# Kernel tuning notes

Hardware: AMD Instinct MI355X
Metric: run time of the kernel (lower is better)

Reference implementation:

```python
import jax, jax.numpy as jnp
import numpy as np

MX, MY, MZ = 16, 16, 8  # modes_x, modes_y, modes_z
B, S1, S2, S3, I = 4, 64, 64, 40, 32
HID = 2 * I  # factor * dim


def setup_inputs() -> dict:
    key = jax.random.key(0)
    ks = jax.random.split(key, 14)
    s = 0.05
    d = {}
    d["x"] = jax.random.normal(ks[0], (B, S1, S2, S3, I), jnp.float32)
    # 1x1 Conv1d (in_dim -> in_dim)
    d["w_weight"] = jax.random.normal(ks[1], (I, I), jnp.float32) * s
    d["w_bias"] = jax.random.normal(ks[2], (I,), jnp.float32) * s
    # fourier_weight (positive-mode blocks), stored as (..., 2) real/imag like torch
    d["fw_xy"] = jax.random.normal(ks[3], (I, I, MX, MY, 2), jnp.float32) * s
    d["fw_yz"] = jax.random.normal(ks[4], (I, I, MY, MZ, 2), jnp.float32) * s
    d["fw_xz"] = jax.random.normal(ks[5], (I, I, MX, MZ, 2), jnp.float32) * s
    # fourier_weight2 (negative-mode blocks)
    d["fw2_xy"] = jax.random.normal(ks[6], (I, I, MX, MY, 2), jnp.float32) * s
    d["fw2_yz"] = jax.random.normal(ks[7], (I, I, MY, MZ, 2), jnp.float32) * s
    d["fw2_xz"] = jax.random.normal(ks[8], (I, I, MX, MZ, 2), jnp.float32) * s
    # backcast FeedForward: Linear(I->2I), ReLU, Linear(2I->I)
    d["ff_w0"] = jax.random.normal(ks[9], (HID, I), jnp.float32) * s
    d["ff_b0"] = jax.random.normal(ks[10], (HID,), jnp.float32) * s
    d["ff_w1"] = jax.random.normal(ks[11], (I, HID), jnp.float32) * s
    d["ff_b1"] = jax.random.normal(ks[12], (I,), jnp.float32) * s
    return d


def _cplx(w):
    return w[..., 0] + 1j * w[..., 1]


def _forward_fourier(x, w_weight, w_bias, fw_xy, fw_yz, fw_xz, fw2_xy, fw2_yz, fw2_xz):
    xt = jnp.transpose(x, (0, 4, 1, 2, 3))  # b i x y z
    b_, i_, s1, s2, s3 = xt.shape
    # 1x1 conv branch
    x_w = jnp.einsum('oi,bixyz->boxyz', w_weight, xt) + w_bias[None, :, None, None, None]
    # --- xz branch: rfftn over (x, z), real axis = z ---
    ft = jnp.fft.rfftn(xt, axes=(-3, -1))          # (b,i,s1,s2,s3//2+1)
    Z = s3 // 2 + 1
    out = jnp.zeros(ft.shape, ft.dtype)
    out = out.at[:, :, :MX, :, :MZ].set(
        jnp.einsum('bixyz,ioxz->boxyz', ft[:, :, :MX, :, :MZ], _cplx(fw_xz)))
    out = out.at[:, :, :MX, :, Z - MZ:].set(
        jnp.einsum('bixyz,ioxz->boxyz', ft[:, :, :MX, :, Z - MZ:], _cplx(fw2_xz)))
    xz = jnp.fft.irfftn(out, s=(s1, s3), axes=(-3, -1))
    # --- yz branch: rfftn over (y, z), real axis = z ---
    ft = jnp.fft.rfftn(xt, axes=(-2, -1))          # (b,i,s1,s2,s3//2+1)
    out = jnp.zeros(ft.shape, ft.dtype)
    out = out.at[:, :, :, :MY, :MZ].set(
        jnp.einsum('bixyz,ioyz->boxyz', ft[:, :, :, :MY, :MZ], _cplx(fw_yz)))
    out = out.at[:, :, :, :MY, Z - MZ:].set(
        jnp.einsum('bixyz,ioyz->boxyz', ft[:, :, :, :MY, Z - MZ:], _cplx(fw2_yz)))
    yz = jnp.fft.irfftn(out, s=(s2, s3), axes=(-2, -1))
    # --- xy branch: rfftn over (x, y), real axis = y ---
    ft = jnp.fft.rfftn(xt, axes=(-3, -2))          # (b,i,s1,s2//2+1,s3)
    Y = s2 // 2 + 1
    out = jnp.zeros(ft.shape, ft.dtype)
    out = out.at[:, :, :MX, :MY, :].set(
        jnp.einsum('bixyz,ioxy->boxyz', ft[:, :, :MX, :MY, :], _cplx(fw_xy)))
    out = out.at[:, :, :MX, Y - MY:, :].set(
        jnp.einsum('bixyz,ioxy->boxyz', ft[:, :, :MX, Y - MY:, :], _cplx(fw2_xy)))
    xy = jnp.fft.irfftn(out, s=(s1, s2), axes=(-3, -2))
    total = xy + yz + xz + x_w
    return jnp.transpose(total, (0, 2, 3, 4, 1))  # b s1 s2 s3 i


def reference(x, w_weight, w_bias, fw_xy, fw_yz, fw_xz, fw2_xy, fw2_yz, fw2_xz,
              ff_w0, ff_b0, ff_w1, ff_b1):
    h = _forward_fourier(x, w_weight, w_bias, fw_xy, fw_yz, fw_xz, fw2_xy, fw2_yz, fw2_xz)
    # backcast FeedForward (dropout=0, no layer_norm): Linear -> ReLU -> Linear
    h1 = jax.nn.relu(h @ ff_w0.T + ff_b0)
    b = h1 @ ff_w1.T + ff_b1
    return b
```

## Files before the change

### kernel.cpp

```cpp
#include <hip/hip_runtime.h>
#include <math.h>

#define TWO_PI 6.28318530717958647692f
#define NXD 64
#define NYD 64
#define NZD 40
#define CID 32
#define NJZ 16
#define NJY 32

#define R1SLOT 2621440ll
#define R2SLOT 655360ll
#define R3SLOT 2621440ll

typedef __attribute__((ext_vector_type(8))) short short8;
typedef __attribute__((ext_vector_type(4))) float float4v;

__device__ inline unsigned short f2bf(float f) {
  unsigned u = __builtin_bit_cast(unsigned, f);
  unsigned r = (u + 0x7fffu + ((u >> 16) & 1u)) >> 16;
  return (unsigned short)r;
}
__device__ inline float bf2f(unsigned short h) {
  return __builtin_bit_cast(float, (unsigned)h << 16);
}

__device__ __align__(16) unsigned short g_invyAH[2][4][64][8];
__device__ __align__(16) unsigned short g_invyAL[2][4][64][8];
__device__ __align__(16) unsigned short g_invzAH[3][64][8];
__device__ __align__(16) unsigned short g_invzAL[3][64][8];
__device__ __align__(16) unsigned short g_fwdyB[2][4][64][8];
__device__ __align__(16) float2 g_ztw[NJZ][NZD];

__global__ __launch_bounds__(256) void k_twprep() {
  int t = threadIdx.x;
  if (blockIdx.x == 0) {
    for (int idx = t; idx < 2 * 4 * 64 * 8; idx += 256) {
      int j = idx & 7, lane = (idx >> 3) & 63, yt = (idx >> 9) & 3, kt = idx >> 11;
      int l15 = lane & 15, quad = lane >> 4;
      int y = yt * 16 + l15;
      int k = kt * 32 + quad * 8 + j;
      int jy = k >> 1, part = k & 1;
      int ky = (jy < 16) ? jy : jy + 1;
      float s_, c_; sincosf(TWO_PI * ((ky * y) & 63) / 64.0f, &s_, &c_);
      float cj = (ky == 0 || ky == 32) ? 1.0f : 2.0f;
      cj *= (1.0f / 4096.0f);
      float val = part ? -cj * s_ : cj * c_;
      unsigned short h = f2bf(val);
      g_invyAH[kt][yt][lane][j] = h;
      g_invyAL[kt][yt][lane][j] = f2bf(val - bf2f(h));
    }
  } else if (blockIdx.x == 1) {
    for (int idx = t; idx < 2 * 4 * 64 * 8; idx += 256) {
      int j = idx & 7, lane = (idx >> 3) & 63, nt = (idx >> 9) & 3, kt = idx >> 11;
      int l15 = lane & 15, quad = lane >> 4;
      int n = nt * 16 + l15;
      int jy = n >> 1, part = n & 1;
      int ky = (jy < 16) ? jy : jy + 1;
      int y = kt * 32 + quad * 8 + j;
      float s_, c_; sincosf(TWO_PI * ((ky * y) & 63) / 64.0f, &s_, &c_);
      g_fwdyB[kt][nt][lane][j] = f2bf(part ? -s_ : c_);
    }
  } else if (blockIdx.x == 2) {
    for (int idx = t; idx < 3 * 64 * 8; idx += 256) {
      int j = idx & 7, lane = (idx >> 3) & 63, zt = idx >> 9;
      int l15 = lane & 15, quad = lane >> 4;
      int z = zt * 16 + l15;
      int k = quad * 8 + j;
      int jz = k >> 1, part = k & 1;
      int kz = (jz < 8) ? jz : jz + 5;
      float s_, c_; sincosf(TWO_PI * ((kz * z) % 40) / 40.0f, &s_, &c_);
      float cj = (kz == 0 || kz == 20) ? 1.0f : 2.0f;
      cj *= (1.0f / 2560.0f);
      float val = part ? -cj * s_ : cj * c_;
      unsigned short h = f2bf(val);
      g_invzAH[zt][lane][j] = h;
      g_invzAL[zt][lane][j] = f2bf(val - bf2f(h));
    }
  } else {
    for (int k = t; k < NJZ * NZD; k += 256) {
      int j = k / NZD, z = k % NZD;
      int kz = (j < 8) ? j : j + 5;
      int m = (kz * z) % NZD;
      float s_, c_; sincosf(TWO_PI * m / (float)NZD, &s_, &c_);
      g_ztw[j][z] = make_float2(c_, -s_);
    }
  }
}

__global__ __launch_bounds__(256) void k_conv_mfma(const float* __restrict__ X,
    const float* __restrict__ Wc, const float* __restrict__ bias,
    float* __restrict__ out) {
  int t = threadIdx.x;
  int wid = t >> 6, lane = t & 63;
  int l15 = lane & 15, quad = lane >> 4;
  short8 B[2];
  float bb[2];
  for (int nt = 0; nt < 2; ++nt) {
    int o = nt * 16 + l15;
    for (int j = 0; j < 8; ++j) B[nt][j] = (short)f2bf(Wc[o * 32 + quad * 8 + j]);
    bb[nt] = bias[o];
  }
  const int TOT = 40960;
  int wg = blockIdx.x * 4 + wid;
  for (int tt = wg; tt < TOT; tt += gridDim.x * 4) {
    long r0 = (long)tt * 16;
    const float4v* p = (const float4v*)(X + (r0 + l15) * 32 + quad * 8);
    float4v x0 = p[0], x1 = p[1];
    short8 a;
    for (int j = 0; j < 4; ++j) { a[j] = (short)f2bf(x0[j]); a[4 + j] = (short)f2bf(x1[j]); }
    for (int nt = 0; nt < 2; ++nt) {
      float4v acc = {0.f, 0.f, 0.f, 0.f};
      acc = __builtin_amdgcn_mfma_f32_16x16x32_bf16(a, B[nt], acc, 0, 0, 0);
      for (int r = 0; r < 4; ++r)
        out[(r0 + quad * 4 + r) * 32 + nt * 16 + l15] = acc[r] + bb[nt];
    }
  }
}

__global__ __launch_bounds__(512) void k_zproj(const float* __restrict__ X,
    float2* __restrict__ Tb, int b0) {
  __shared__ float xs[4][NZD][CID];
  __shared__ float2 tw[NJZ][NZD];
  int t = threadIdx.x;
  int xy0 = blockIdx.x * 4;
  int b = b0 + blockIdx.z;
  float2* T = Tb + (long)blockIdx.z * R1SLOT;
  const float4v* src = (const float4v*)(X + ((long)(b * 4096 + xy0)) * NZD * CID);
  float4v* xsf = (float4v*)&xs[0][0][0];
  for (int k = t; k < 1280; k += 512) xsf[k] = src[k];
  {
    const float2* gt = &g_ztw[0][0];
    for (int k = t; k < NJZ * NZD; k += 512) tw[k / NZD][k % NZD] = gt[k];
  }
  __syncthreads();
  int j = t >> 5, i = t & 31;
  float2 acc0 = make_float2(0.f, 0.f), acc1 = make_float2(0.f, 0.f);
  float2 acc2 = make_float2(0.f, 0.f), acc3 = make_float2(0.f, 0.f);
  for (int z = 0; z < NZD; ++z) {
    float2 w = tw[j][z];
    float v0 = xs[0][z][i], v1 = xs[1][z][i], v2 = xs[2][z][i], v3 = xs[3][z][i];
    acc0.x += v0 * w.x; acc0.y += v0 * w.y;
    acc1.x += v1 * w.x; acc1.y += v1 * w.y;
    acc2.x += v2 * w.x; acc2.y += v2 * w.y;
    acc3.x += v3 * w.x; acc3.y += v3 * w.y;
  }
  T[((long)(xy0 + 0) * NJZ + j) * CID + i] = acc0;
  T[((long)(xy0 + 1) * NJZ + j) * CID + i] = acc1;
  T[((long)(xy0 + 2) * NJZ + j) * CID + i] = acc2;
  T[((long)(xy0 + 3) * NJZ + j) * CID + i] = acc3;
}

__global__ __launch_bounds__(256) void k_fwddft(const float2* __restrict__ inb,
    float2* __restrict__ Ub, long CS, long SS, long JS) {
  __shared__ float2 tw[64];
  int t = threadIdx.x;
  if (t < 64) {
    float s_, c_; sincosf(TWO_PI * t / 64.0f, &s_, &c_);
    tw[t] = make_float2(c_, -s_);
  }
  int j = blockIdx.x >> 1, mh = blockIdx.x & 1, sc = blockIdx.y;
  int J = gridDim.x >> 1, SD = gridDim.y * 8;
  int m0 = mh * 8;
  int s = sc * 8 + (t >> 5), i = t & 31;
  const float2* in = inb + (long)blockIdx.z * R1SLOT + (long)j * JS + (long)s * SS + i;
  float2 acc[8];
#pragma unroll
  for (int m = 0; m < 8; ++m) acc[m] = make_float2(0.f, 0.f);
  __syncthreads();
#pragma unroll 4
  for (int c = 0; c < 64; ++c) {
    float2 v = in[(long)c * CS];
#pragma unroll
    for (int m = 0; m < 8; ++m) {
      float2 w = tw[((m0 + m) * c) & 63];
      acc[m].x += v.x * w.x - v.y * w.y;
      acc[m].y += v.x * w.y + v.y * w.x;
    }
  }
  float2* U = Ub + (long)blockIdx.z * R3SLOT;
#pragma unroll
  for (int m = 0; m < 8; ++m)
    U[((long)((m0 + m) * J + j) * SD + s) * 32 + i] = acc[m];
}

__global__ __launch_bounds__(256) void k_mix(const float2* __restrict__ Ub,
    float2* __restrict__ Vb, const float* __restrict__ fw, const float* __restrict__ fw2,
    int jsplit, int JW, long OM, long OJ, long OS, int SD) {
  __shared__ float2 Us[64][32];
  __shared__ float2 Wm[32][32];
  int m = blockIdx.x, j = blockIdx.y, t = threadIdx.x;
  int J = gridDim.y;
  const float2* U = Ub + (long)blockIdx.z * R3SLOT + (long)(m * J + j) * SD * 32;
  for (int k = t; k < SD * 32; k += 256) Us[k >> 5][k & 31] = U[k];
  {
    const float* src = (j < jsplit) ? fw : fw2;
    int jl = (j < jsplit) ? j : j - jsplit;
    for (int k = t; k < 1024; k += 256) {
      int i = k >> 5, o = k & 31;
      const float* p = src + (((i * 32 + o) * 16 + m) * JW + jl) * 2;
      Wm[i][o] = make_float2(p[0], p[1]);
    }
  }
  __syncthreads();
  int o = t & 31, sg = t >> 5;
  float2* V = Vb + (long)blockIdx.z * R2SLOT;
  for (int s = sg; s < SD; s += 8) {
    float2 acc = make_float2(0.f, 0.f);
    for (int i2 = 0; i2 < 32; ++i2) {
      float2 u = Us[s][i2], w = Wm[i2][o];
      acc.x += u.x * w.x - u.y * w.y;
      acc.y += u.x * w.y + u.y * w.x;
    }
    V[(long)m * OM + (long)j * OJ + (long)s * OS + o] = acc;
  }
}

__global__ __launch_bounds__(256) void k_invaxis(const float2* __restrict__ Vb,
    float2* __restrict__ Pb) {
  __shared__ float2 Vs[16][CID];
  __shared__ float2 twp[64];
  int s = blockIdx.x, j = blockIdx.y, t = threadIdx.x;
  const float2* V = Vb + (long)blockIdx.z * R2SLOT;
  float2* P = Pb + (long)blockIdx.z * R3SLOT;
  if (t < 64) {
    float s_, c_; sincosf(TWO_PI * t / 64.0f, &s_, &c_);
    twp[t] = make_float2(c_, s_);
  }
  for (int k = t; k < 512; k += 256) {
    int mm = k >> 5, o = k & 31;
    Vs[mm][o] = V[((long)(mm * 64 + s) * NJZ + j) * CID + o];
  }
  __syncthreads();
  int o = t & 31, vg = t >> 5;
  for (int k = 0; k < 8; ++k) {
    int v = vg + 8 * k;
    float2 acc = make_float2(0.f, 0.f);
    for (int mm = 0; mm < 16; ++mm) {
      float2 w = twp[(mm * v) & 63];
      float2 vv = Vs[mm][o];
      acc.x += vv.x * w.x - vv.y * w.y;
      acc.y += vv.x * w.y + vv.y * w.x;
    }
    P[((long)(v * 64 + s) * NJZ + j) * CID + o] = acc;
  }
}

__global__ __launch_bounds__(256) void k_invzadd_mfma(const float2* __restrict__ Pb,
    float* __restrict__ out, long strideV, long strideS, int b0) {
  __shared__ __align__(16) char smem[21504];
  unsigned (*PsH)[21] = (unsigned(*)[21])smem;
  unsigned (*PsL)[21] = (unsigned(*)[21])(smem + 10752);
  float (*Cs)[132] = (float(*)[132])smem;
  int t = threadIdx.x;
  int wid = t >> 6, lane = t & 63;
  int l15 = lane & 15, quad = lane >> 4;
  int b = b0 + blockIdx.z;
  int vv = blockIdx.y;
  int s0 = blockIdx.x * 4;
  short8 AH[3], AL[3];
  for (int zt = 0; zt < 3; ++zt) {
    AH[zt] = *(const short8*)&g_invzAH[zt][lane][0];
    AL[zt] = *(const short8*)&g_invzAL[zt][lane][0];
  }
  const float2* src = Pb + (long)blockIdx.z * R3SLOT + ((long)(vv * 64 + s0) * NJZ) * CID;
  for (int kk = t; kk < 16 * 128; kk += 256) {
    int j = kk >> 7, m = kk & 127;
    int sl = m >> 5, o = m & 31;
    float2 v = src[((long)sl * NJZ + j) * CID + o];
    unsigned short hx = f2bf(v.x), hy = f2bf(v.y);
    unsigned short lx = f2bf(v.x - bf2f(hx)), ly = f2bf(v.y - bf2f(hy));
    PsH[m][j] = (unsigned)hx | ((unsigned)hy << 16);
    PsL[m][j] = (unsigned)lx | ((unsigned)ly << 16);
  }
  __syncthreads();
  short8 bh[2], bl[2];
  for (int mt = 0; mt < 2; ++mt) {
    int mc = wid * 32 + mt * 16 + l15;
    union { unsigned u[4]; short8 s; } th, tl;
    for (int c = 0; c < 4; ++c) {
      th.u[c] = PsH[mc][quad * 4 + c];
      tl.u[c] = PsL[mc][quad * 4 + c];
    }
    bh[mt] = th.s; bl[mt] = tl.s;
  }
  __syncthreads();
  for (int mt = 0; mt < 2; ++mt) {
    int mc = wid * 32 + mt * 16;
    for (int zt = 0; zt < 3; ++zt) {
      float4v acc = {0.f, 0.f, 0.f, 0.f};
      acc = __builtin_amdgcn_mfma_f32_16x16x32_bf16(AL[zt], bh[mt], acc, 0, 0, 0);
      acc = __builtin_amdgcn_mfma_f32_16x16x32_bf16(AH[zt], bl[mt], acc, 0, 0, 0);
      acc = __builtin_amdgcn_mfma_f32_16x16x32_bf16(AH[zt], bh[mt], acc, 0, 0, 0);
      for (int r = 0; r < 4; ++r) {
        int z = zt * 16 + quad * 4 + r;
        if (z < 40) Cs[z][mc + l15] = acc[r];
      }
    }
  }
  __syncthreads();
  float* obb = out + (long)b * (NXD * NYD * NZD * CID) + (long)vv * strideV
             + (long)s0 * strideS;
  for (int idx = t; idx < 4 * 40 * 8; idx += 256) {
    int sl = idx / 320, rem = idx - sl * 320;
    int z = rem >> 3, o4 = rem & 7;
    float4v* gp = (float4v*)(obb + (long)sl * strideS + z * 32 + o4 * 4);
    float4v g = *gp;
    float4v c = *(const float4v*)&Cs[z][sl * 32 + o4 * 4];
    g.x += c.x; g.y += c.y; g.z += c.z; g.w += c.w;
    *gp = g;
  }
}

__global__ __launch_bounds__(256) void k_fwdy_mfma(const float* __restrict__ X,
    float2* __restrict__ Sb, int b0) {
  __shared__ __align__(16) char smem[35328];
  unsigned (*Xs)[37] = (unsigned(*)[37])smem;
  float (*Cs)[69] = (float(*)[69])smem;
  int t = threadIdx.x;
  int wid = t >> 6, lane = t & 63;
  int l15 = lane & 15, quad = lane >> 4;
  int b = b0 + blockIdx.z;
  int x = blockIdx.y;
  int m0 = blockIdx.x * 128;
  short8 Bf[2][4];
  for (int kt = 0; kt < 2; ++kt)
    for (int nt = 0; nt < 4; ++nt)
      Bf[kt][nt] = *(const short8*)&g_fwdyB[kt][nt][lane][0];
  const float* src = X + (((long)b * 64 + x) * 64) * 1280 + m0;
  for (int k = t; k < 32 * 128; k += 256) {
    int y2 = k >> 7, m = k & 127;
    float v0 = src[(long)(2 * y2) * 1280 + m];
    float v1 = src[(long)(2 * y2 + 1) * 1280 + m];
    Xs[m][y2] = (unsigned)f2bf(v0) | ((unsigned)f2bf(v1) << 16);
  }
  __syncthreads();
  short8 a[2][2];
  for (int mt = 0; mt < 2; ++mt) {
    int mrow = wid * 32 + mt * 16 + l15;
    for (int kt = 0; kt < 2; ++kt) {
      union { unsigned u[4]; short8 s; } tmp;
      for (int c = 0; c < 4; ++c) tmp.u[c] = Xs[mrow][kt * 16 + quad * 4 + c];
      a[mt][kt] = tmp.s;
    }
  }
  __syncthreads();
  for (int mt = 0; mt < 2; ++mt) {
    for (int nt = 0; nt < 4; ++nt) {
      float4v acc = {0.f, 0.f, 0.f, 0.f};
      acc = __builtin_amdgcn_mfma_f32_16x16x32_bf16(a[mt][0], Bf[0][nt], acc, 0, 0, 0);
      acc = __builtin_amdgcn_mfma_f32_16x16x32_bf16(a[mt][1], Bf[1][nt], acc, 0, 0, 0);
      int n = nt * 16 + l15;
      for (int r = 0; r < 4; ++r)
        Cs[wid * 32 + mt * 16 + quad * 4 + r][n] = acc[r];
    }
  }
  __syncthreads();
  float2* S = Sb + (long)blockIdx.z * R1SLOT + (long)x * (NJY * NZD * CID) + m0;
  for (int idx = t; idx < 32 * 128; idx += 256) {
    int jy = idx >> 7, m = idx & 127;
    S[(long)jy * 1280 + m] = make_float2(Cs[m][2 * jy], Cs[m][2 * jy + 1]);
  }
}

__global__ __launch_bounds__(256) void k_invx_xy(const float2* __restrict__ V2b,
    float2* __restrict__ P2b) {
  __shared__ float2 Vs[16][CID];
  __shared__ float2 twp[64];
  int jy = blockIdx.x, z = blockIdx.y, t = threadIdx.x;
  const float2* V2 = V2b + (long)blockIdx.z * R2SLOT;
  float2* P2 = P2b + (long)blockIdx.z * R3SLOT;
  if (t < 64) {
    float s_, c_; sincosf(TWO_PI * t / 64.0f, &s_, &c_);
    twp[t] = make_float2(c_, s_);
  }
  for (int k = t; k < 512; k += 256) {
    int kx = k >> 5, o = k & 31;
    Vs[kx][o] = V2[(((long)kx * NJY + jy) * NZD + z) * CID + o];
  }
  __syncthreads();
  int o = t & 31, xg = t >> 5;
  for (int k = 0; k < 8; ++k) {
    int x = xg + 8 * k;
    float2 acc = make_float2(0.f, 0.f);
    for (int kx = 0; kx < 16; ++kx) {
      float2 w = twp[(kx * x) & 63];
      float2 v = Vs[kx][o];
      acc.x += v.x * w.x - v.y * w.y;
      acc.y += v.x * w.y + v.y * w.x;
    }
    P2[(((long)x * NJY + jy) * NZD + z) * CID + o] = acc;
  }
}

__global__ __launch_bounds__(256) void k_invyadd_mfma(const float2* __restrict__ P2b,
    float* __restrict__ out, int b0) {
  __shared__ __align__(16) char smem[18944];
  unsigned (*PsH)[37] = (unsigned(*)[37])smem;
  unsigned (*PsL)[37] = (unsigned(*)[37])(smem + 9472);
  float (*Cs)[68] = (float(*)[68])smem;
  int t = threadIdx.x;
  int wid = t >> 6, lane = t & 63;
  int l15 = lane & 15, quad = lane >> 4;
  int b = b0 + blockIdx.z;
  int x = blockIdx.y;
  int m0 = blockIdx.x * 64;
  const float2* src = P2b + (long)blockIdx.z * R3SLOT + (long)x * (NJY * NZD * CID) + m0;
  for (int kk = t; kk < 32 * 64; kk += 256) {
    int jy = kk >> 6, m = kk & 63;
    float2 v = src[(long)jy * (NZD * CID) + m];
    unsigned short hx = f2bf(v.x), hy = f2bf(v.y);
    unsigned short lx = f2bf(v.x - bf2f(hx)), ly = f2bf(v.y - bf2f(hy));
    PsH[m][jy] = (unsigned)hx | ((unsigned)hy << 16);
    PsL[m][jy] = (unsigned)lx | ((unsigned)ly << 16);
  }
  __syncthreads();
  int mc = wid * 16;
  short8 bh0, bh1, bl0, bl1;
  {
    union { unsigned u[4]; short8 s; } t0, t1, t2, t3;
    for (int c = 0; c < 4; ++c) {
      t0.u[c] = PsH[mc + l15][quad * 4 + c];
      t1.u[c] = PsH[mc + l15][16 + quad * 4 + c];
      t2.u[c] = PsL[mc + l15][quad * 4 + c];
      t3.u[c] = PsL[mc + l15][16 + quad * 4 + c];
    }
    bh0 = t0.s; bh1 = t1.s; bl0 = t2.s; bl1 = t3.s;
  }
  __syncthreads();
#pragma unroll 1
  for (int yt = 0; yt < 4; ++yt) {
    short8 AH0 = *(const short8*)&g_invyAH[0][yt][lane][0];
    short8 AH1 = *(const short8*)&g_invyAH[1][yt][lane][0];
    short8 AL0 = *(const short8*)&g_invyAL[0][yt][lane][0];
    short8 AL1 = *(const short8*)&g_invyAL[1][yt][lane][0];
    float4v acc = {0.f, 0.f, 0.f, 0.f};
    acc = __builtin_amdgcn_mfma_f32_16x16x32_bf16(AL0, bh0, acc, 0, 0, 0);
    acc = __builtin_amdgcn_mfma_f32_16x16x32_bf16(AL1, bh1, acc, 0, 0, 0);
    acc = __builtin_amdgcn_mfma_f32_16x16x32_bf16(AH0, bl0, acc, 0, 0, 0);
    acc = __builtin_amdgcn_mfma_f32_16x16x32_bf16(AH1, bl1, acc, 0, 0, 0);
    acc = __builtin_amdgcn_mfma_f32_16x16x32_bf16(AH0, bh0, acc, 0, 0, 0);
    acc = __builtin_amdgcn_mfma_f32_16x16x32_bf16(AH1, bh1, acc, 0, 0, 0);
    for (int r = 0; r < 4; ++r) {
      int y = yt * 16 + quad * 4 + r;
      Cs[y][mc + l15] = acc[r];
    }
  }
  __syncthreads();
  float* ob = out + ((long)(b * 64 + x)) * (NYD * NZD * CID) + m0;
  for (int idx = t; idx < 64 * 16; idx += 256) {
    int y = idx >> 4, f = idx & 15;
    float4v* gp = (float4v*)(ob + (long)y * (NZD * CID) + f * 4);
    float4v g = *gp;
    float4v c = *(const float4v*)&Cs[y][f * 4];
    g.x += c.x; g.y += c.y; g.z += c.z; g.w += c.w;
    *gp = g;
  }
}

__global__ __launch_bounds__(256) void k_ff_mfma(float* __restrict__ out,
    const float* __restrict__ W0, const float* __restrict__ b0,
    const float* __restrict__ W1, const float* __restrict__ b1) {
  __shared__ unsigned short h1s[4][16 * 64];
  int t = threadIdx.x;
  int wid = t >> 6, lane = t & 63;
  int l15 = lane & 15, quad = lane >> 4;
  short8 B1[4];
  float bb0[4];
  for (int nt = 0; nt < 4; ++nt) {
    int hh = nt * 16 + l15;
    for (int j = 0; j < 8; ++j) B1[nt][j] = (short)f2bf(W0[hh * 32 + quad * 8 + j]);
    bb0[nt] = b0[hh];
  }
  short8 B2[2][2];
  float bb1[2];
  for (int k0 = 0; k0 < 2; ++k0)
    for (int nt = 0; nt < 2; ++nt) {
      int o = nt * 16 + l15;
      for (int j = 0; j < 8; ++j)
        B2[k0][nt][j] = (short)f2bf(W1[o * 64 + k0 * 32 + quad * 8 + j]);
    }
  for (int nt = 0; nt < 2; ++nt) bb1[nt] = b1[nt * 16 + l15];

  const int TOT = 40960;
  int wg = blockIdx.x * 4 + wid;
  unsigned short* hs = h1s[wid];
  for (int tt = wg; tt < TOT; tt += gridDim.x * 4) {
    long r0 = (long)tt * 16;
    const float4v* p = (const float4v*)(out + (r0 + l15) * 32 + quad * 8);
    float4v x0 = p[0], x1 = p[1];
    short8 a1;
    for (int j = 0; j < 4; ++j) { a1[j] = (short)f2bf(x0[j]); a1[4 + j] = (short)f2bf(x1[j]); }
    for (int nt = 0; nt < 4; ++nt) {
      float4v acc = {0.f, 0.f, 0.f, 0.f};
      acc = __builtin_amdgcn_mfma_f32_16x16x32_bf16(a1, B1[nt], acc, 0, 0, 0);
      for (int r = 0; r < 4; ++r) {
        float v = acc[r] + bb0[nt];
        v = v > 0.f ? v : 0.f;
        hs[(quad * 4 + r) * 64 + nt * 16 + l15] = f2bf(v);
      }
    }
    short8 a2[2];
    for (int k0 = 0; k0 < 2; ++k0)
      a2[k0] = *(const short8*)&hs[l15 * 64 + k0 * 32 + quad * 8];
    for (int nt = 0; nt < 2; ++nt) {
      float4v acc = {0.f, 0.f, 0.f, 0.f};
      acc = __builtin_amdgcn_mfma_f32_16x16x32_bf16(a2[0], B2[0][nt], acc, 0, 0, 0);
      acc = __builtin_amdgcn_mfma_f32_16x16x32_bf16(a2[1], B2[1][nt], acc, 0, 0, 0);
      for (int r = 0; r < 4; ++r)
        out[(r0 + quad * 4 + r) * 32 + nt * 16 + l15] = acc[r] + bb1[nt];
    }
  }
}

extern "C" void kernel_launch(void* const* d_in, const int* in_sizes, int n_in,
                              void* d_out, int out_size, void* d_ws, size_t ws_size,
                              hipStream_t stream) {
  const float* X       = (const float*)d_in[0];
  const float* w_w     = (const float*)d_in[1];
  const float* w_b     = (const float*)d_in[2];
  const float* fw_xy   = (const float*)d_in[3];
  const float* fw_yz   = (const float*)d_in[4];
  const float* fw_xz   = (const float*)d_in[5];
  const float* fw2_xy  = (const float*)d_in[6];
  const float* fw2_yz  = (const float*)d_in[7];
  const float* fw2_xz  = (const float*)d_in[8];
  const float* ff_w0   = (const float*)d_in[9];
  const float* ff_b0   = (const float*)d_in[10];
  const float* ff_w1   = (const float*)d_in[11];
  const float* ff_b1   = (const float*)d_in[12];
  float* out = (float*)d_out;
  char* ws = (char*)d_ws;

  const size_t need_full = (size_t)(R1SLOT + R2SLOT + R3SLOT) * 4 * 8;
  bool full = ws_size >= need_full;

  float2 *r1, *r2, *r3;
  if (full) {
    r1 = (float2*)ws;
    r2 = (float2*)(ws + (size_t)R1SLOT * 4 * 8);
    r3 = (float2*)(ws + (size_t)(R1SLOT + R2SLOT) * 4 * 8);
  } else {
    r1 = (float2*)ws;
    r2 = (float2*)(ws + (size_t)R1SLOT * 8);
    r3 = (float2*)(ws + (size_t)(R1SLOT + R2SLOT) * 8);
  }

  k_twprep<<<dim3(4), dim3(256), 0, stream>>>();
  k_conv_mfma<<<dim3(2560), dim3(256), 0, stream>>>(X, w_w, w_b, out);

  int nz = full ? 4 : 1;
  int nb = full ? 1 : 4;
  for (int b = 0; b < nb; ++b) {
    k_zproj<<<dim3(1024, 1, nz), dim3(512), 0, stream>>>(X, r1, b);
    k_fwddft<<<dim3(32, 8, nz), dim3(256), 0, stream>>>(r1, r3, 32768, 512, 32);
    k_mix<<<dim3(16, 16, nz), dim3(256), 0, stream>>>(r3, r2, fw_xz, fw2_xz,
        8, 8, 32768, 32, 512, 64);
    k_invaxis<<<dim3(64, 16, nz), dim3(256), 0, stream>>>(r2, r3);
    k_invzadd_mfma<<<dim3(16, 64, nz), dim3(256), 0, stream>>>(r3, out, 64 * 40 * 32, 40 * 32, b);
    k_fwddft<<<dim3(32, 8, nz), dim3(256), 0, stream>>>(r1, r3, 512, 32768, 32);
    k_mix<<<dim3(16, 16, nz), dim3(256), 0, stream>>>(r3, r2, fw_yz, fw2_yz,
        8, 8, 32768, 32, 512, 64);
    k_invaxis<<<dim3(64, 16, nz), dim3(256), 0, stream>>>(r2, r3);
    k_invzadd_mfma<<<dim3(16, 64, nz), dim3(256), 0, stream>>>(r3, out, 40 * 32, 64 * 40 * 32, b);
    k_fwdy_mfma<<<dim3(10, 64, nz), dim3(256), 0, stream>>>(X, r1, b);
    k_fwddft<<<dim3(64, 5, nz), dim3(256), 0, stream>>>(r1, r3, 40960, 32, 1280);
    k_mix<<<dim3(16, 32, nz), dim3(256), 0, stream>>>(r3, r2, fw_xy, fw2_xy,
        16, 16, 40960, 1280, 32, 40);
    k_invx_xy<<<dim3(32, 40, nz), dim3(256), 0, stream>>>(r2, r3);
    k_invyadd_mfma<<<dim3(20, 64, nz), dim3(256), 0, stream>>>(r3, out, b);
  }

  k_ff_mfma<<<dim3(2560), dim3(256), 0, stream>>>(out, ff_w0, ff_b0, ff_w1, ff_b1);
}
```

Before: 728.0 us.

## Fuse xz and yz inverse-z transforms with 1x1 conv into one kernel

Removes the standalone 1x1 conv kernel and the two separate inverse-z kernels that read-modify-wrote the output. A single kernel now loads both the xz and yz spectra, accumulates them in the same MFMA chain, adds the bf16 conv of X plus bias, and writes the output once. To keep both intermediates alive, the yz branch buffers are moved into unused space in the r1 workspace slot, and the per-slot strides become kernel parameters. This cuts several full passes over the output array, at the cost of more LDS and register pressure per block.

```diff
diff --git a/kernel.cpp b/kernel.cpp
--- a/kernel.cpp
+++ b/kernel.cpp
@@ -12,6 +12,7 @@
 #define R1SLOT 2621440ll
 #define R2SLOT 655360ll
 #define R3SLOT 2621440ll
+#define PYZ_UOFF 2097152ll
 
 typedef __attribute__((ext_vector_type(8))) short short8;
 typedef __attribute__((ext_vector_type(4))) float float4v;
@@ -88,36 +89,6 @@
   }
 }
 
-__global__ __launch_bounds__(256) void k_conv_mfma(const float* __restrict__ X,
-    const float* __restrict__ Wc, const float* __restrict__ bias,
-    float* __restrict__ out) {
-  int t = threadIdx.x;
-  int wid = t >> 6, lane = t & 63;
-  int l15 = lane & 15, quad = lane >> 4;
-  short8 B[2];
-  float bb[2];
-  for (int nt = 0; nt < 2; ++nt) {
-    int o = nt * 16 + l15;
-    for (int j = 0; j < 8; ++j) B[nt][j] = (short)f2bf(Wc[o * 32 + quad * 8 + j]);
-    bb[nt] = bias[o];
-  }
-  const int TOT = 40960;
-  int wg = blockIdx.x * 4 + wid;
-  for (int tt = wg; tt < TOT; tt += gridDim.x * 4) {
-    long r0 = (long)tt * 16;
-    const float4v* p = (const float4v*)(X + (r0 + l15) * 32 + quad * 8);
-    float4v x0 = p[0], x1 = p[1];
-    short8 a;
-    for (int j = 0; j < 4; ++j) { a[j] = (short)f2bf(x0[j]); a[4 + j] = (short)f2bf(x1[j]); }
-    for (int nt = 0; nt < 2; ++nt) {
-      float4v acc = {0.f, 0.f, 0.f, 0.f};
-      acc = __builtin_amdgcn_mfma_f32_16x16x32_bf16(a, B[nt], acc, 0, 0, 0);
-      for (int r = 0; r < 4; ++r)
-        out[(r0 + quad * 4 + r) * 32 + nt * 16 + l15] = acc[r] + bb[nt];
-    }
-  }
-}
-
 __global__ __launch_bounds__(512) void k_zproj(const float* __restrict__ X,
     float2* __restrict__ Tb, int b0) {
   __shared__ float xs[4][NZD][CID];
@@ -152,7 +123,7 @@
 }
 
 __global__ __launch_bounds__(256) void k_fwddft(const float2* __restrict__ inb,
-    float2* __restrict__ Ub, long CS, long SS, long JS) {
+    float2* __restrict__ Ub, long CS, long SS, long JS, long inSlot, long uSlot) {
   __shared__ float2 tw[64];
   int t = threadIdx.x;
   if (t < 64) {
@@ -163,7 +134,7 @@
   int J = gridDim.x >> 1, SD = gridDim.y * 8;
   int m0 = mh * 8;
   int s = sc * 8 + (t >> 5), i = t & 31;
-  const float2* in = inb + (long)blockIdx.z * R1SLOT + (long)j * JS + (long)s * SS + i;
+  const float2* in = inb + (long)blockIdx.z * inSlot + (long)j * JS + (long)s * SS + i;
   float2 acc[8];
 #pragma unroll
   for (int m = 0; m < 8; ++m) acc[m] = make_float2(0.f, 0.f);
@@ -178,7 +149,7 @@
       acc[m].y += v.x * w.y + v.y * w.x;
     }
   }
-  float2* U = Ub + (long)blockIdx.z * R3SLOT;
+  float2* U = Ub + (long)blockIdx.z * uSlot;
 #pragma unroll
   for (int m = 0; m < 8; ++m)
     U[((long)((m0 + m) * J + j) * SD + s) * 32 + i] = acc[m];
@@ -186,12 +157,12 @@
 
 __global__ __launch_bounds__(256) void k_mix(const float2* __restrict__ Ub,
     float2* __restrict__ Vb, const float* __restrict__ fw, const float* __restrict__ fw2,
-    int jsplit, int JW, long OM, long OJ, long OS, int SD) {
+    int jsplit, int JW, long OM, long OJ, long OS, int SD, long uSlot) {
   __shared__ float2 Us[64][32];
   __shared__ float2 Wm[32][32];
   int m = blockIdx.x, j = blockIdx.y, t = threadIdx.x;
   int J = gridDim.y;
-  const float2* U = Ub + (long)blockIdx.z * R3SLOT + (long)(m * J + j) * SD * 32;
+  const float2* U = Ub + (long)blockIdx.z * uSlot + (long)(m * J + j) * SD * 32;
   for (int k = t; k < SD * 32; k += 256) Us[k >> 5][k & 31] = U[k];
   {
     const float* src = (j < jsplit) ? fw : fw2;
@@ -217,12 +188,12 @@
 }
 
 __global__ __launch_bounds__(256) void k_invaxis(const float2* __restrict__ Vb,
-    float2* __restrict__ Pb) {
+    float2* __restrict__ Pb, long pSlot) {
   __shared__ float2 Vs[16][CID];
   __shared__ float2 twp[64];
   int s = blockIdx.x, j = blockIdx.y, t = threadIdx.x;
   const float2* V = Vb + (long)blockIdx.z * R2SLOT;
-  float2* P = Pb + (long)blockIdx.z * R3SLOT;
+  float2* P = Pb + (long)blockIdx.z * pSlot;
   if (t < 64) {
     float s_, c_; sincosf(TWO_PI * t / 64.0f, &s_, &c_);
     twp[t] = make_float2(c_, s_);
@@ -246,9 +217,12 @@
   }
 }
 
-__global__ __launch_bounds__(256) void k_invzadd_mfma(const float2* __restrict__ Pb,
-    float* __restrict__ out, long strideV, long strideS, int b0) {
+__global__ __launch_bounds__(256) void k_invzz_conv(
+    const float2* __restrict__ Pxz, const float2* __restrict__ Pyz,
+    const float* __restrict__ X, const float* __restrict__ Wc,
+    const float* __restrict__ bias, float* __restrict__ out, int b0) {
   __shared__ __align__(16) char smem[21504];
+  __shared__ __align__(16) unsigned short Xbf[160][36];
   unsigned (*PsH)[21] = (unsigned(*)[21])smem;
   unsigned (*PsL)[21] = (unsigned(*)[21])(smem + 10752);
   float (*Cs)[132] = (float(*)[132])smem;
@@ -263,35 +237,71 @@
     AH[zt] = *(const short8*)&g_invzAH[zt][lane][0];
     AL[zt] = *(const short8*)&g_invzAL[zt][lane][0];
   }
-  const float2* src = Pb + (long)blockIdx.z * R3SLOT + ((long)(vv * 64 + s0) * NJZ) * CID;
-  for (int kk = t; kk < 16 * 128; kk += 256) {
-    int j = kk >> 7, m = kk & 127;
-    int sl = m >> 5, o = m & 31;
-    float2 v = src[((long)sl * NJZ + j) * CID + o];
+  short8 Bc[2]; float bb[2];
+  for (int nt = 0; nt < 2; ++nt) {
+    int o = nt * 16 + l15;
+    for (int j = 0; j < 8; ++j) Bc[nt][j] = (short)f2bf(Wc[o * 32 + quad * 8 + j]);
+    bb[nt] = bias[o];
+  }
+  const float2* src1 = Pxz + (long)blockIdx.z * R3SLOT + ((long)(vv * 64 + s0) * NJZ) * CID;
+  for (int kk = t; kk < 2048; kk += 256) {
+    int j = kk >> 7, m = kk & 127, sl = m >> 5, o = m & 31;
+    float2 v = src1[((long)sl * NJZ + j) * CID + o];
     unsigned short hx = f2bf(v.x), hy = f2bf(v.y);
     unsigned short lx = f2bf(v.x - bf2f(hx)), ly = f2bf(v.y - bf2f(hy));
     PsH[m][j] = (unsigned)hx | ((unsigned)hy << 16);
     PsL[m][j] = (unsigned)lx | ((unsigned)ly << 16);
   }
-  __syncthreads();
-  short8 bh[2], bl[2];
+  const float4v* xsrc = (const float4v*)(X + ((long)(b * 4096 + vv * 64 + s0)) * NZD * CID);
+  for (int e4 = t; e4 < 1280; e4 += 256) {
+    float4v v = xsrc[e4];
+    int row = e4 >> 3, c0 = (e4 & 7) * 4;
+    *(unsigned*)&Xbf[row][c0]     = (unsigned)f2bf(v.x) | ((unsigned)f2bf(v.y) << 16);
+    *(unsigned*)&Xbf[row][c0 + 2] = (unsigned)f2bf(v.z) | ((unsigned)f2bf(v.w) << 16);
+  }
+  __syncthreads();
+  short8 bhx[2], blx[2];
   for (int mt = 0; mt < 2; ++mt) {
     int mc = wid * 32 + mt * 16 + l15;
     union { unsigned u[4]; short8 s; } th, tl;
-    for (int c = 0; c < 4; ++c) {
-      th.u[c] = PsH[mc][quad * 4 + c];
-      tl.u[c] = PsL[mc][quad * 4 + c];
-    }
-    bh[mt] = th.s; bl[mt] = tl.s;
+    for (int c = 0; c < 4; ++c) { th.u[c] = PsH[mc][quad * 4 + c]; tl.u[c] = PsL[mc][quad * 4 + c]; }
+    bhx[mt] = th.s; blx[mt] = tl.s;
+  }
+  __syncthreads();
+  const float2* src2 = Pyz + (long)blockIdx.z * R1SLOT + ((long)(s0 * 64 + vv) * NJZ) * CID;
+  for (int kk = t; kk < 2048; kk += 256) {
+    int j = kk >> 7, m = kk & 127, sl = m >> 5, o = m & 31;
+    float2 v = src2[(long)sl * (64 * NJZ * CID) + j * CID + o];
+    unsigned short hx = f2bf(v.x), hy = f2bf(v.y);
+    unsigned short lx = f2bf(v.x - bf2f(hx)), ly = f2bf(v.y - bf2f(hy));
+    PsH[m][j] = (unsigned)hx | ((unsigned)hy << 16);
+    PsL[m][j] = (unsigned)lx | ((unsigned)ly << 16);
+  }
+  __syncthreads();
+  short8 bhy[2], bly[2];
+  for (int mt = 0; mt < 2; ++mt) {
+    int mc = wid * 32 + mt * 16 + l15;
+    union { unsigned u[4]; short8 s; } th, tl;
+    for (int c = 0; c < 4; ++c) { th.u[c] = PsH[mc][quad * 4 + c]; tl.u[c] = PsL[mc][quad * 4 + c]; }
+    bhy[mt] = th.s; bly[mt] = tl.s;
+  }
+  short8 ca[3];
+  int ntile = (wid < 2) ? 3 : 2;
+  for (int u = 0; u < ntile; ++u) {
+    int row = (wid + u * 4) * 16 + l15;
+    ca[u] = *(const short8*)&Xbf[row][quad * 8];
   }
   __syncthreads();
   for (int mt = 0; mt < 2; ++mt) {
     int mc = wid * 32 + mt * 16;
     for (int zt = 0; zt < 3; ++zt) {
       float4v acc = {0.f, 0.f, 0.f, 0.f};
-      acc = __builtin_amdgcn_mfma_f32_16x16x32_bf16(AL[zt], bh[mt], acc, 0, 0, 0);
-      acc = __builtin_amdgcn_mfma_f32_16x16x32_bf16(AH[zt], bl[mt], acc, 0, 0, 0);
-      acc = __builtin_amdgcn_mfma_f32_16x16x32_bf16(AH[zt], bh[mt], acc, 0, 0, 0);
+      acc = __builtin_amdgcn_mfma_f32_16x16x32_bf16(AL[zt], bhx[mt], acc, 0, 0, 0);
+      acc = __builtin_amdgcn_mfma_f32_16x16x32_bf16(AH[zt], blx[mt], acc, 0, 0, 0);
+      acc = __builtin_amdgcn_mfma_f32_16x16x32_bf16(AH[zt], bhx[mt], acc, 0, 0, 0);
+      acc = __builtin_amdgcn_mfma_f32_16x16x32_bf16(AL[zt], bhy[mt], acc, 0, 0, 0);
+      acc = __builtin_amdgcn_mfma_f32_16x16x32_bf16(AH[zt], bly[mt], acc, 0, 0, 0);
+      acc = __builtin_amdgcn_mfma_f32_16x16x32_bf16(AH[zt], bhy[mt], acc, 0, 0, 0);
       for (int r = 0; r < 4; ++r) {
         int z = zt * 16 + quad * 4 + r;
         if (z < 40) Cs[z][mc + l15] = acc[r];
@@ -299,16 +309,26 @@
     }
   }
   __syncthreads();
-  float* obb = out + (long)b * (NXD * NYD * NZD * CID) + (long)vv * strideV
-             + (long)s0 * strideS;
-  for (int idx = t; idx < 4 * 40 * 8; idx += 256) {
+  for (int u = 0; u < ntile; ++u) {
+    int tile = wid + u * 4;
+    for (int nt = 0; nt < 2; ++nt) {
+      float4v acc = {0.f, 0.f, 0.f, 0.f};
+      acc = __builtin_amdgcn_mfma_f32_16x16x32_bf16(ca[u], Bc[nt], acc, 0, 0, 0);
+      for (int r = 0; r < 4; ++r) {
+        int rg = tile * 16 + quad * 4 + r;
+        int sl = rg / NZD, z = rg % NZD;
+        Cs[z][sl * 32 + nt * 16 + l15] += acc[r] + bb[nt];
+      }
+    }
+  }
+  __syncthreads();
+  float* obb = out + (long)b * (NXD * NYD * NZD * CID)
+             + (long)vv * (NYD * NZD * CID) + (long)s0 * (NZD * CID);
+  for (int idx = t; idx < 1280; idx += 256) {
     int sl = idx / 320, rem = idx - sl * 320;
     int z = rem >> 3, o4 = rem & 7;
-    float4v* gp = (float4v*)(obb + (long)sl * strideS + z * 32 + o4 * 4);
-    float4v g = *gp;
-    float4v c = *(const float4v*)&Cs[z][sl * 32 + o4 * 4];
-    g.x += c.x; g.y += c.y; g.z += c.z; g.w += c.w;
-    *gp = g;
+    *(float4v*)(obb + (long)sl * (NZD * CID) + z * 32 + o4 * 4) =
+        *(const float4v*)&Cs[z][sl * 32 + o4 * 4];
   }
 }
 
@@ -547,26 +567,27 @@
   }
 
   k_twprep<<<dim3(4), dim3(256), 0, stream>>>();
-  k_conv_mfma<<<dim3(2560), dim3(256), 0, stream>>>(X, w_w, w_b, out);
 
   int nz = full ? 4 : 1;
   int nb = full ? 1 : 4;
   for (int b = 0; b < nb; ++b) {
     k_zproj<<<dim3(1024, 1, nz), dim3(512), 0, stream>>>(X, r1, b);
-    k_fwddft<<<dim3(32, 8, nz), dim3(256), 0, stream>>>(r1, r3, 32768, 512, 32);
+    k_fwddft<<<dim3(32, 8, nz), dim3(256), 0, stream>>>(r1, r3, 32768, 512, 32,
+        R1SLOT, R3SLOT);
     k_mix<<<dim3(16, 16, nz), dim3(256), 0, stream>>>(r3, r2, fw_xz, fw2_xz,
-        8, 8, 32768, 32, 512, 64);
-    k_invaxis<<<dim3(64, 16, nz), dim3(256), 0, stream>>>(r2, r3);
-    k_invzadd_mfma<<<dim3(16, 64, nz), dim3(256), 0, stream>>>(r3, out, 64 * 40 * 32, 40 * 32, b);
-    k_fwddft<<<dim3(32, 8, nz), dim3(256), 0, stream>>>(r1, r3, 512, 32768, 32);
-    k_mix<<<dim3(16, 16, nz), dim3(256), 0, stream>>>(r3, r2, fw_yz, fw2_yz,
-        8, 8, 32768, 32, 512, 64);
-    k_invaxis<<<dim3(64, 16, nz), dim3(256), 0, stream>>>(r2, r3);
-    k_invzadd_mfma<<<dim3(16, 64, nz), dim3(256), 0, stream>>>(r3, out, 40 * 32, 64 * 40 * 32, b);
+        8, 8, 32768, 32, 512, 64, R3SLOT);
+    k_invaxis<<<dim3(64, 16, nz), dim3(256), 0, stream>>>(r2, r3, R3SLOT);
+    k_fwddft<<<dim3(32, 8, nz), dim3(256), 0, stream>>>(r1, r1 + PYZ_UOFF,
+        512, 32768, 32, R1SLOT, R1SLOT);
+    k_mix<<<dim3(16, 16, nz), dim3(256), 0, stream>>>(r1 + PYZ_UOFF, r2, fw_yz, fw2_yz,
+        8, 8, 32768, 32, 512, 64, R1SLOT);
+    k_invaxis<<<dim3(64, 16, nz), dim3(256), 0, stream>>>(r2, r1, R1SLOT);
+    k_invzz_conv<<<dim3(16, 64, nz), dim3(256), 0, stream>>>(r3, r1, X, w_w, w_b, out, b);
     k_fwdy_mfma<<<dim3(10, 64, nz), dim3(256), 0, stream>>>(X, r1, b);
-    k_fwddft<<<dim3(64, 5, nz), dim3(256), 0, stream>>>(r1, r3, 40960, 32, 1280);
+    k_fwddft<<<dim3(64, 5, nz), dim3(256), 0, stream>>>(r1, r3, 40960, 32, 1280,
+        R1SLOT, R3SLOT);
     k_mix<<<dim3(16, 32, nz), dim3(256), 0, stream>>>(r3, r2, fw_xy, fw2_xy,
-        16, 16, 40960, 1280, 32, 40);
+        16, 16, 40960, 1280, 32, 40, R3SLOT);
     k_invx_xy<<<dim3(32, 40, nz), dim3(256), 0, stream>>>(r2, r3);
     k_invyadd_mfma<<<dim3(20, 64, nz), dim3(256), 0, stream>>>(r3, out, b);
   }
```

Measured after the change: 741.4 us. Within noise of the previous version (+1.8%).
